# Performance work log

Hardware: AMD Instinct MI355X
Metric: run time of the kernel (lower is better)

Reference implementation:

```python
import jax, jax.numpy as jnp
import numpy as np

B, TOK, D, H, L = 64, 20, 512, 8, 4
S = 512          # tokens per half
HD = D // H
ODIM = 32        # encoder_output_dim


def _ln(x, g, b):
    m = x.mean(-1, keepdims=True)
    v = ((x - m) ** 2).mean(-1, keepdims=True)
    return (x - m) / jnp.sqrt(v + 1e-5) * g + b


def _alibi_slopes(h):
    # mirrors FlashAttentionBlock.build_alibi_slopes (base=2.0)
    base = 2.0
    return jnp.asarray([1.0 / base ** (i // (h // base)) for i in range(h)], dtype=jnp.float32)


def setup_inputs() -> dict:
    key = jax.random.key(0)
    ks = jax.random.split(key, 16)
    r = lambda i, shape, s=0.02: jax.random.normal(ks[i], shape, jnp.float32) * s
    return {
        'x': jax.random.normal(ks[0], (B, 2 * S * TOK), jnp.float32),
        'in_W': r(1, (TOK, D)), 'in_b': jnp.zeros((D,)),
        'qkv_W': r(2, (L, D, 3 * D)), 'qkv_b': jnp.zeros((L, 3 * D)),
        'ln1_g': jnp.ones((L, D)), 'ln1_b': jnp.zeros((L, D)),
        'ffn_W1': r(3, (L, D, 4 * D)), 'ffn_b1': jnp.zeros((L, 4 * D)),
        'ffn_W2': r(4, (L, 4 * D, D)), 'ffn_b2': jnp.zeros((L, D)),
        'ln2_g': jnp.ones((L, D)), 'ln2_b': jnp.zeros((L, D)),
        'out_W': r(5, (D, ODIM)), 'out_b': jnp.zeros((ODIM,)),
        'd1_W': r(6, (2 * S * ODIM, 256)), 'd1_b': jnp.zeros((256,)),
        'bn1_g': jnp.ones((256,)), 'bn1_b': jnp.zeros((256,)),
        'bn1_m': jnp.zeros((256,)), 'bn1_v': jnp.ones((256,)),
        'd2_W': r(7, (256, 128)), 'd2_b': jnp.zeros((128,)),
        'bn2_g': jnp.ones((128,)), 'bn2_b': jnp.zeros((128,)),
        'bn2_m': jnp.zeros((128,)), 'bn2_v': jnp.ones((128,)),
        'fin_W': r(8, (128, 1)), 'fin_b': jnp.zeros((1,)),
    }


def _forward(x, in_W, in_b, qkv_W, qkv_b, ln1_g, ln1_b, ffn_W1, ffn_b1,
             ffn_W2, ffn_b2, ln2_g, ln2_b, out_W, out_b,
             d1_W, d1_b, bn1_g, bn1_b, bn1_m, bn1_v,
             d2_W, d2_b, bn2_g, bn2_b, bn2_m, bn2_v, fin_W, fin_b):
    slopes = _alibi_slopes(H)                                   # [H]
    pos = jnp.arange(S)
    # non-causal ALiBi bias: -slope * |i - j|, shape [H, S, S]
    bias = -slopes[:, None, None] * jnp.abs(pos[:, None] - pos[None, :]).astype(jnp.float32)
    scale = 1.0 / np.sqrt(HD).astype(np.float32)

    def encode(xh):
        b = xh.shape[0]
        t = xh.reshape(b, S, TOK) @ in_W + in_b                 # [b, S, D]
        for l in range(L):
            res = t
            qkv = (t @ qkv_W[l] + qkv_b[l]).reshape(b, S, 3, H, HD)
            q, k, v = qkv[:, :, 0], qkv[:, :, 1], qkv[:, :, 2]  # [b, S, H, HD]
            scores = jnp.einsum('bqhd,bkhd->bhqk', q, k) * scale + bias[None]
            attn = jax.nn.softmax(scores, axis=-1)
            o = jnp.einsum('bhqk,bkhd->bqhd', attn, v).reshape(b, S, D)
            t = _ln(res + o, ln1_g[l], ln1_b[l])
            res = t
            f = jax.nn.relu(t @ ffn_W1[l] + ffn_b1[l]) @ ffn_W2[l] + ffn_b2[l]
            t = _ln(res + f, ln2_g[l], ln2_b[l])
        return (t @ out_W + out_b).reshape(b, -1)               # [b, S*ODIM]

    half = S * TOK
    h = jnp.concatenate([encode(x[:, :half]), encode(x[:, half:])], axis=-1)
    bn = lambda z, g, bb, m, v: (z - m) / jnp.sqrt(v + 1e-5) * g + bb
    h = bn(jax.nn.relu(h @ d1_W + d1_b), bn1_g, bn1_b, bn1_m, bn1_v)
    h = bn(jax.nn.relu(h @ d2_W + d2_b), bn2_g, bn2_b, bn2_m, bn2_v)
    return (h @ fin_W + fin_b).squeeze(-1)                      # [B]


def reference(x, in_W, in_b, qkv_W, qkv_b, ln1_g, ln1_b, ffn_W1, ffn_b1,
              ffn_W2, ffn_b2, ln2_g, ln2_b, out_W, out_b,
              d1_W, d1_b, bn1_g, bn1_b, bn1_m, bn1_v,
              d2_W, d2_b, bn2_g, bn2_b, bn2_m, bn2_v, fin_W, fin_b):
    return _forward(x, in_W, in_b, qkv_W, qkv_b, ln1_g, ln1_b, ffn_W1, ffn_b1,
                    ffn_W2, ffn_b2, ln2_g, ln2_b, out_W, out_b,
                    d1_W, d1_b, bn1_g, bn1_b, bn1_m, bn1_v,
                    d2_W, d2_b, bn2_g, bn2_b, bn2_m, bn2_v, fin_W, fin_b)
```

## Files before the change

kernel.cpp:

```cpp
#include <hip/hip_runtime.h>

#define DEV __device__ __forceinline__

using bf16x8 = __attribute__((ext_vector_type(8))) __bf16;
using f32x4  = __attribute__((ext_vector_type(4))) float;
using u16x8  = __attribute__((ext_vector_type(8))) unsigned short;
using u16x4  = __attribute__((ext_vector_type(4))) unsigned short;

DEV unsigned short f2bf(float f) {
  unsigned u = __builtin_bit_cast(unsigned, f);
  u += 0x7fffu + ((u >> 16) & 1u);
  return (unsigned short)(u >> 16);
}
DEV float bf2f(unsigned short h) {
  unsigned u = ((unsigned)h) << 16;
  return __builtin_bit_cast(float, u);
}
DEV f32x4 mfma16(u16x8 a, u16x8 b, f32x4 c) {
  return __builtin_amdgcn_mfma_f32_16x16x32_bf16(
      __builtin_bit_cast(bf16x8, a), __builtin_bit_cast(bf16x8, b), c, 0, 0, 0);
}
DEV f32x4 zero4() { f32x4 z = {0.f, 0.f, 0.f, 0.f}; return z; }

DEV void glds16(const unsigned short* g, unsigned short* l) {
  __builtin_amdgcn_global_load_lds(
      (const __attribute__((address_space(1))) unsigned int*)g,
      (__attribute__((address_space(3))) unsigned int*)l, 16, 0, 0);
}

#define PH_BAR()                          \
  do {                                    \
    __builtin_amdgcn_sched_barrier(0);    \
    __builtin_amdgcn_s_barrier();         \
    __builtin_amdgcn_sched_barrier(0);    \
  } while (0)

enum { EPI_BIAS = 0, EPI_RELU = 1, EPI_OUT = 2 };

template <int EPI>
__global__ __launch_bounds__(512, 2) void gemm32_k(
    const unsigned short* __restrict__ A, const unsigned short* __restrict__ Bt,
    const float* __restrict__ bias, unsigned short* __restrict__ C, int N, int K) {
  __shared__ unsigned short As[2][8192];
  __shared__ unsigned short Bs[2][8192];
  const int tid = threadIdx.x;
  const int lane = tid & 63, wv = tid >> 6;
  const int q = lane >> 4, ln = lane & 15;
  const int wr = wv >> 2, wc = wv & 3;
  const int ln3 = ln & 3;

  const int Nt = gridDim.x, Mt = gridDim.y;
  const int lin = blockIdx.x + Nt * blockIdx.y;
  const int xcd = lin & 7;
  const int j = lin >> 3;
  const int mi = xcd * (Mt >> 3) + j / Nt;
  const int ni = j % Nt;
  const int m0 = mi << 8, n0 = ni << 8;

  f32x4 acc[8][4];
#pragma unroll
  for (int i = 0; i < 8; ++i)
#pragma unroll
    for (int jj = 0; jj < 4; ++jj) acc[i][jj] = zero4();

  const int sr = lane >> 2;
  const int sc = ((lane & 3) ^ (sr & 3)) << 3;
  const unsigned short* Abase = A + (size_t)(m0 + wv * 16 + sr) * K + sc;
  const unsigned short* Bbase = Bt + (size_t)(n0 + wv * 16 + sr) * K + sc;

  const int T = K >> 5;

  auto stA = [&](int buf, int t) {
    unsigned short* d = &As[buf][wv * 512];
    const unsigned short* s = Abase + t * 32;
    glds16(s, d);
    glds16(s + (size_t)128 * K, d + 4096);
  };
  auto stB = [&](int buf, int t) {
    unsigned short* d = &Bs[buf][wv * 512];
    const unsigned short* s = Bbase + t * 32;
    glds16(s, d);
    glds16(s + (size_t)128 * K, d + 4096);
  };

  stA(0, 0);
  stB(0, 0);
  if (T > 1) {
    stA(1, 1);
    stB(1, 1);
    asm volatile("s_waitcnt vmcnt(4)" ::: "memory");
  } else {
    asm volatile("s_waitcnt vmcnt(0)" ::: "memory");
  }
  PH_BAR();

  for (int u = 0; u < T; ++u) {
    const int cur = u & 1;
    const unsigned short* Ab = &As[cur][0];
    const unsigned short* Bb = &Bs[cur][0];
    u16x8 a0[4], a1[4], b0[4];

#pragma unroll
    for (int mt = 0; mt < 4; ++mt)
      a0[mt] = *(const u16x8*)(Ab + (wr * 128 + mt * 16 + ln) * 32 + ((q ^ ln3) << 3));
#pragma unroll
    for (int nt = 0; nt < 4; ++nt)
      b0[nt] = *(const u16x8*)(Bb + (wc * 64 + nt * 16 + ln) * 32 + ((q ^ ln3) << 3));
    PH_BAR();
    __builtin_amdgcn_s_setprio(1);
#pragma unroll
    for (int nt = 0; nt < 4; ++nt)
#pragma unroll
      for (int mt = 0; mt < 4; ++mt) acc[mt][nt] = mfma16(a0[mt], b0[nt], acc[mt][nt]);
    __builtin_amdgcn_s_setprio(0);
    PH_BAR();

#pragma unroll
    for (int mt = 0; mt < 4; ++mt)
      a1[mt] = *(const u16x8*)(Ab + (wr * 128 + (mt + 4) * 16 + ln) * 32 + ((q ^ ln3) << 3));
    if (u + 2 < T) stB(cur, u + 2);
    PH_BAR();
    __builtin_amdgcn_s_setprio(1);
#pragma unroll
    for (int nt = 0; nt < 4; ++nt)
#pragma unroll
      for (int mt = 0; mt < 4; ++mt)
        acc[mt + 4][nt] = mfma16(a1[mt], b0[nt], acc[mt + 4][nt]);
    __builtin_amdgcn_s_setprio(0);
    PH_BAR();

    if (u + 1 < T) {
      if (u + 2 < T) {
        stA(cur, u + 2);
        asm volatile("s_waitcnt vmcnt(4)" ::: "memory");
      } else {
        asm volatile("s_waitcnt vmcnt(0)" ::: "memory");
      }
      PH_BAR();
    }
  }

#pragma unroll
  for (int mt = 0; mt < 8; ++mt) {
    const int rowb = m0 + wr * 128 + mt * 16 + q * 4;
#pragma unroll
    for (int nt = 0; nt < 4; ++nt) {
      const int col = n0 + wc * 64 + nt * 16 + ln;
      const float bs = bias[col];
#pragma unroll
      for (int r = 0; r < 4; ++r) {
        float v = acc[mt][nt][r] + bs;
        if (EPI == EPI_RELU) v = fmaxf(v, 0.f);
        C[(size_t)(rowb + r) * N + col] = f2bf(v);
      }
    }
  }
}

template <int EPI>
__global__ __launch_bounds__(256) void gemm_k(
    const unsigned short* __restrict__ A, const unsigned short* __restrict__ Bt,
    const float* __restrict__ bias, unsigned short* __restrict__ C, int N, int K) {
  __shared__ unsigned short As[128 * 64];
  __shared__ unsigned short Bs[128 * 64];
  const int tid = threadIdx.x;
  const int lane = tid & 63, wv = tid >> 6;
  const int q = lane >> 4, ln = lane & 15;
  const int wr = wv >> 1, wc = wv & 1;

  const int Nt = gridDim.x, Mt = gridDim.y;
  const int lin = blockIdx.x + Nt * blockIdx.y;
  const int xcd = lin & 7;
  const int j = lin >> 3;
  const int mi = xcd * (Mt >> 3) + j / Nt;
  const int ni = j % Nt;
  const int m0 = mi << 7, n0 = ni << 7;

  f32x4 acc[4][4];
#pragma unroll
  for (int i = 0; i < 4; ++i)
#pragma unroll
    for (int jj = 0; jj < 4; ++jj) acc[i][jj] = zero4();

  const int ra = lane >> 3;
  const int ca = ((lane & 7) ^ ra) << 3;
  const unsigned short* Ap = A + (size_t)(m0 + wv * 32 + ra) * K + ca;
  const unsigned short* Bp = Bt + (size_t)(n0 + wv * 32 + ra) * K + ca;
  unsigned short* AsW = As + wv * 2048;
  unsigned short* BsW = Bs + wv * 2048;
  const int ln7 = ln & 7;

  for (int kb = 0; kb < K; kb += 64) {
    __syncthreads();
#pragma unroll
    for (int t = 0; t < 4; ++t) {
      glds16(Ap + (size_t)(t * 8) * K + kb, AsW + t * 512);
      glds16(Bp + (size_t)(t * 8) * K + kb, BsW + t * 512);
    }
    __syncthreads();
#pragma unroll
    for (int kk = 0; kk < 2; ++kk) {
      const int c = kk * 4 + q;
      const int lo = ln * 64 + ((c ^ ln7) << 3);
      u16x8 af[4];
#pragma unroll
      for (int mt = 0; mt < 4; ++mt)
        af[mt] = *(const u16x8*)(As + (wr * 64 + mt * 16) * 64 + lo);
#pragma unroll
      for (int nt = 0; nt < 4; ++nt) {
        u16x8 bf = *(const u16x8*)(Bs + (wc * 64 + nt * 16) * 64 + lo);
#pragma unroll
        for (int mt = 0; mt < 4; ++mt) acc[mt][nt] = mfma16(af[mt], bf, acc[mt][nt]);
      }
    }
  }

#pragma unroll
  for (int mt = 0; mt < 4; ++mt) {
    const int rowb = m0 + wr * 64 + mt * 16 + q * 4;
#pragma unroll
    for (int nt = 0; nt < 4; ++nt) {
      const int col = n0 + wc * 64 + nt * 16 + ln;
      if (EPI == EPI_OUT && col >= 32) continue;
      const float bs = bias[col];
      const int ldc = (EPI == EPI_OUT) ? 32 : N;
#pragma unroll
      for (int r = 0; r < 4; ++r) {
        float v = acc[mt][nt][r] + bs;
        if (EPI == EPI_RELU) v = fmaxf(v, 0.f);
        C[(size_t)(rowb + r) * ldc + col] = f2bf(v);
      }
    }
  }
}

__global__ __launch_bounds__(256) void vt_k(const unsigned short* __restrict__ big,
                                            unsigned short* __restrict__ vt) {
  __shared__ unsigned short td[64 * 72];
  const int tid = threadIdx.x;
  const int sh = blockIdx.x;
  const int seq = sh >> 3, h = sh & 7;
  const int kt = blockIdx.y;
  {
    const int key = tid >> 2, hdc = (tid & 3) << 4;
    const unsigned short* src =
        big + ((size_t)seq * 512 + kt * 64 + key) * 1536 + 1024 + h * 64 + hdc;
    *(u16x8*)(td + key * 72 + hdc) = *(const u16x8*)src;
    *(u16x8*)(td + key * 72 + hdc + 8) = *(const u16x8*)(src + 8);
  }
  __syncthreads();
  {
    const int hd = tid >> 2, kc = (tid & 3) << 4;
    u16x8 a, b;
#pragma unroll
    for (int j = 0; j < 8; ++j) a[j] = td[(kc + j) * 72 + hd];
#pragma unroll
    for (int j = 0; j < 8; ++j) b[j] = td[(kc + 8 + j) * 72 + hd];
    unsigned short* dst = vt + ((size_t)sh * 64 + hd) * 512 + kt * 64 + kc;
    *(u16x8*)dst = a;
    *(u16x8*)(dst + 8) = b;
  }
}

__global__ __launch_bounds__(256) void attn_k(const unsigned short* __restrict__ qkv,
                                              const unsigned short* __restrict__ vt,
                                              unsigned short* __restrict__ o) {
  __shared__ unsigned short Qs[128 * 72];
  __shared__ unsigned short Ks[2][64 * 64];
  __shared__ unsigned short Vts[2][64 * 64];
  unsigned short* Ps = Qs;
  const int tid = threadIdx.x;
  const int lane = tid & 63, w = tid >> 6, q = lane >> 4, ln = lane & 15;
  const int bh = blockIdx.x;
  const int seq = bh >> 3, h = bh & 7;
  const int qt = blockIdx.y;
  const size_t tokb = (size_t)seq * 512;
  const int qoff = h * 64, koff = 512 + h * 64;
  const float c1 = 0.125f * 1.44269504f;
  const float c2 = ((h < 4) ? 1.0f : 0.5f) * 1.44269504f;

#pragma unroll
  for (int p = 0; p < 4; ++p) {
    int c = p * 256 + tid;
    int row = c >> 3, cc = (c & 7) << 3;
    u16x8 v = *(const u16x8*)(qkv + (tokb + qt * 128 + row) * 1536 + qoff + cc);
    *(u16x8*)(Qs + row * 72 + cc) = v;
  }

  const int sr = lane >> 3;
  const int sc = ((lane & 7) ^ sr) << 3;
  const unsigned short* Kp = qkv + (tokb + w * 16 + sr) * 1536 + koff + sc;
  const unsigned short* Vp = vt + ((size_t)bh * 64 + w * 16 + sr) * 512 + sc;
  const int ln7 = ln & 7;

  auto stage = [&](int kt, int buf) {
    unsigned short* KsW = &Ks[buf][w * 1024];
    unsigned short* VsW = &Vts[buf][w * 1024];
    glds16(Kp + (size_t)(kt * 64) * 1536, KsW);
    glds16(Kp + (size_t)(kt * 64 + 8) * 1536, KsW + 512);
    glds16(Vp + kt * 64, VsW);
    glds16(Vp + kt * 64 + (size_t)8 * 512, VsW + 512);
  };

  stage(0, 0);

  __syncthreads();
  u16x8 aq[2][2];
#pragma unroll
  for (int mt = 0; mt < 2; ++mt)
#pragma unroll
    for (int kc = 0; kc < 2; ++kc)
      aq[mt][kc] = *(const u16x8*)(Qs + (w * 32 + mt * 16 + ln) * 72 + kc * 32 + q * 8);

  float lacc[2] = {0.f, 0.f};
  f32x4 o_acc[2][4];
#pragma unroll
  for (int mt = 0; mt < 2; ++mt)
#pragma unroll
    for (int ht = 0; ht < 4; ++ht) o_acc[mt][ht] = zero4();

  for (int kt = 0; kt < 8; ++kt) {
    const int buf = kt & 1;
    __syncthreads();
    if (kt + 1 < 8) {
      stage(kt + 1, buf ^ 1);
      asm volatile("s_waitcnt vmcnt(4)" ::: "memory");
    } else {
      asm volatile("s_waitcnt vmcnt(0)" ::: "memory");
    }
    __builtin_amdgcn_sched_barrier(0);
    __builtin_amdgcn_s_barrier();
    __builtin_amdgcn_sched_barrier(0);

    f32x4 sacc[2][4];
#pragma unroll
    for (int mt = 0; mt < 2; ++mt)
#pragma unroll
      for (int nt = 0; nt < 4; ++nt) sacc[mt][nt] = zero4();
#pragma unroll
    for (int nt = 0; nt < 4; ++nt)
#pragma unroll
      for (int kc = 0; kc < 2; ++kc) {
        u16x8 bk = *(const u16x8*)(&Ks[buf][(nt * 16 + ln) * 64 + (((kc * 4 + q) ^ ln7) << 3)]);
#pragma unroll
        for (int mt = 0; mt < 2; ++mt) sacc[mt][nt] = mfma16(bk, aq[mt][kc], sacc[mt][nt]);
      }

    const float qp0 = (float)(qt * 128 + w * 32 + ln);
    const float kb0 = (float)(kt * 64 + q * 4);
#pragma unroll
    for (int mt = 0; mt < 2; ++mt) {
      const float qpm = qp0 + (float)(mt * 16);
#pragma unroll
      for (int nt = 0; nt < 4; ++nt) {
        const float kp = kb0 + (float)(nt * 16);
        u16x4 pk;
#pragma unroll
        for (int r = 0; r < 4; ++r) {
          const float ad = fabsf(qpm - (kp + (float)r));
          const float p = exp2f(fmaf(sacc[mt][nt][r], c1, -c2 * ad));
          const unsigned u = __builtin_bit_cast(unsigned, p);
          const unsigned short pb = (unsigned short)((u + 0x8000u) >> 16);
          pk[r] = pb;
          lacc[mt] += bf2f(pb);
        }
        *(u16x4*)(Ps + (w * 32 + mt * 16 + ln) * 72 + nt * 16 + q * 4) = pk;
      }
    }
#pragma unroll
    for (int kc = 0; kc < 2; ++kc) {
      u16x8 pa[2];
#pragma unroll
      for (int mt = 0; mt < 2; ++mt)
        pa[mt] = *(const u16x8*)(Ps + (w * 32 + mt * 16 + ln) * 72 + kc * 32 + q * 8);
#pragma unroll
      for (int ht = 0; ht < 4; ++ht) {
        u16x8 bv = *(const u16x8*)(&Vts[buf][(ht * 16 + ln) * 64 + (((kc * 4 + q) ^ ln7) << 3)]);
#pragma unroll
        for (int mt = 0; mt < 2; ++mt) o_acc[mt][ht] = mfma16(pa[mt], bv, o_acc[mt][ht]);
      }
    }
  }

  float rl[2][4];
#pragma unroll
  for (int mt = 0; mt < 2; ++mt) {
    float l = lacc[mt];
    l += __shfl_xor(l, 16, 64);
    l += __shfl_xor(l, 32, 64);
    const int sb = (lane >> 4) * 20;
#pragma unroll
    for (int r = 0; r < 4; ++r) rl[mt][r] = 1.0f / __shfl(l, sb + r, 64);
  }

#pragma unroll
  for (int mt = 0; mt < 2; ++mt)
#pragma unroll
    for (int ht = 0; ht < 4; ++ht)
#pragma unroll
      for (int r = 0; r < 4; ++r) {
        const int row = qt * 128 + w * 32 + mt * 16 + q * 4 + r;
        const float val = o_acc[mt][ht][r] * rl[mt][r];
        o[(tokb + row) * 512 + h * 64 + ht * 16 + ln] = f2bf(val);
      }
}

__global__ __launch_bounds__(256) void ln_k(const unsigned short* res,
                                            const unsigned short* __restrict__ y,
                                            const float* __restrict__ g,
                                            const float* __restrict__ b,
                                            unsigned short* out) {
  const int lane = threadIdx.x & 63, wv = threadIdx.x >> 6;
  const size_t row = (size_t)blockIdx.x * 4 + wv;
  const size_t base = row * 512 + lane * 8;
  u16x8 rv = *(const u16x8*)(res + base);
  u16x8 yv = *(const u16x8*)(y + base);
  float v[8];
  float s = 0.f, s2 = 0.f;
#pragma unroll
  for (int i = 0; i < 8; ++i) {
    v[i] = bf2f(rv[i]) + bf2f(yv[i]);
    s += v[i];
    s2 += v[i] * v[i];
  }
#pragma unroll
  for (int m = 1; m < 64; m <<= 1) {
    s += __shfl_xor(s, m, 64);
    s2 += __shfl_xor(s2, m, 64);
  }
  const float mean = s * (1.f / 512.f);
  const float var = s2 * (1.f / 512.f) - mean * mean;
  const float rstd = rsqrtf(var + 1e-5f);
  const int c = lane * 8;
  u16x8 ov;
#pragma unroll
  for (int i = 0; i < 8; ++i) ov[i] = f2bf((v[i] - mean) * rstd * g[c + i] + b[c + i]);
  *(u16x8*)(out + base) = ov;
}

__global__ __launch_bounds__(256) void transpose_w(const float* __restrict__ in,
                                                   unsigned short* __restrict__ out,
                                                   int Kin, int Nin, int Kout, int Nout) {
  __shared__ float tile[32][33];
  const int nb = blockIdx.x * 32, kb = blockIdx.y * 32;
  const int tx = threadIdx.x & 31, ty = threadIdx.x >> 5;
#pragma unroll
  for (int i = 0; i < 32; i += 8) {
    int k = kb + ty + i, n = nb + tx;
    tile[ty + i][tx] = (k < Kin && n < Nin) ? in[(size_t)k * Nin + n] : 0.f;
  }
  __syncthreads();
#pragma unroll
  for (int i = 0; i < 32; i += 8) {
    int n = nb + ty + i, k = kb + tx;
    if (n < Nout && k < Kout) out[(size_t)n * Kout + k] = f2bf(tile[tx][ty + i]);
  }
}

__global__ __launch_bounds__(256) void xpad_k(const float* __restrict__ x,
                                              unsigned short* __restrict__ xp) {
  const int idx = blockIdx.x * 256 + threadIdx.x;
  const int tok = idx >> 6, k = idx & 63;
  const int seq = tok >> 9, s = tok & 511;
  const int hf = seq >> 6, b = seq & 63;
  float v = 0.f;
  if (k < 20) v = x[(size_t)b * 20480 + hf * 10240 + s * 20 + k];
  xp[idx] = f2bf(v);
}

__global__ __launch_bounds__(256) void d1_part(const unsigned short* __restrict__ enc,
                                               const float* __restrict__ W,
                                               float* __restrict__ pz) {
  __shared__ float ef[64 * 128];
  const int tid = threadIdx.x;
  const int kb = blockIdx.x * 128;
  const int hf = kb >> 14;
  const int j0 = kb & 16383;
  {
    const int m = tid >> 2, c = (tid & 3) * 32;
    const unsigned short* src = enc + (size_t)hf * 1048576 + (size_t)m * 16384 + j0 + c;
#pragma unroll
    for (int i = 0; i < 4; ++i) {
      u16x8 v = *(const u16x8*)(src + i * 8);
#pragma unroll
      for (int jj = 0; jj < 8; ++jj) ef[m * 128 + c + i * 8 + jj] = bf2f(v[jj]);
    }
  }
  __syncthreads();
  const int n = tid;
  float acc[64];
#pragma unroll
  for (int m = 0; m < 64; ++m) acc[m] = 0.f;
  for (int kc = 0; kc < 128; kc += 4) {
    const float w0 = W[(size_t)(kb + kc) * 256 + n];
    const float w1 = W[(size_t)(kb + kc + 1) * 256 + n];
    const float w2 = W[(size_t)(kb + kc + 2) * 256 + n];
    const float w3 = W[(size_t)(kb + kc + 3) * 256 + n];
#pragma unroll
    for (int m = 0; m < 64; ++m) {
      const f32x4 e = *(const f32x4*)(ef + m * 128 + kc);
      acc[m] += e[0] * w0 + e[1] * w1 + e[2] * w2 + e[3] * w3;
    }
  }
#pragma unroll
  for (int m = 0; m < 64; ++m)
    pz[(size_t)(blockIdx.x * 64 + m) * 256 + n] = acc[m];
}

__global__ __launch_bounds__(256) void d1_fin(const float* __restrict__ pz,
                                              const float* __restrict__ d1b,
                                              const float* __restrict__ g,
                                              const float* __restrict__ b,
                                              const float* __restrict__ mm,
                                              const float* __restrict__ vv,
                                              float* __restrict__ h1) {
  const int m = blockIdx.x, n = threadIdx.x;
  float a = d1b[n];
  for (int sl = 0; sl < 256; ++sl) a += pz[(size_t)(sl * 64 + m) * 256 + n];
  a = fmaxf(a, 0.f);
  a = (a - mm[n]) * rsqrtf(vv[n] + 1e-5f) * g[n] + b[n];
  h1[m * 256 + n] = a;
}

__global__ __launch_bounds__(128) void d2_k(const float* __restrict__ h1,
                                            const float* __restrict__ W,
                                            const float* __restrict__ bb,
                                            const float* __restrict__ g,
                                            const float* __restrict__ b,
                                            const float* __restrict__ mm,
                                            const float* __restrict__ vv,
                                            float* __restrict__ h2) {
  __shared__ float hs[256];
  const int m = blockIdx.x, n = threadIdx.x;
  hs[n] = h1[m * 256 + n];
  hs[n + 128] = h1[m * 256 + n + 128];
  __syncthreads();
  float a = bb[n];
#pragma unroll 8
  for (int k = 0; k < 256; ++k) a += hs[k] * W[k * 128 + n];
  a = fmaxf(a, 0.f);
  a = (a - mm[n]) * rsqrtf(vv[n] + 1e-5f) * g[n] + b[n];
  h2[m * 128 + n] = a;
}

__global__ __launch_bounds__(64) void fin_k(const float* __restrict__ h2,
                                            const float* __restrict__ W,
                                            const float* __restrict__ fb,
                                            float* __restrict__ out) {
  const int m = threadIdx.x;
  float a = fb[0];
#pragma unroll 8
  for (int k = 0; k < 128; ++k) a += h2[m * 128 + k] * W[k];
  out[m] = a;
}

extern "C" void kernel_launch(void* const* d_in, const int* in_sizes, int n_in,
                              void* d_out, int out_size, void* d_ws, size_t ws_size,
                              hipStream_t stream) {
  const float* x      = (const float*)d_in[0];
  const float* in_W   = (const float*)d_in[1];
  const float* in_b   = (const float*)d_in[2];
  const float* qkv_W  = (const float*)d_in[3];
  const float* qkv_b  = (const float*)d_in[4];
  const float* ln1_g  = (const float*)d_in[5];
  const float* ln1_b  = (const float*)d_in[6];
  const float* ffn_W1 = (const float*)d_in[7];
  const float* ffn_b1 = (const float*)d_in[8];
  const float* ffn_W2 = (const float*)d_in[9];
  const float* ffn_b2 = (const float*)d_in[10];
  const float* ln2_g  = (const float*)d_in[11];
  const float* ln2_b  = (const float*)d_in[12];
  const float* out_W  = (const float*)d_in[13];
  const float* out_b  = (const float*)d_in[14];
  const float* d1W    = (const float*)d_in[15];
  const float* d1b    = (const float*)d_in[16];
  const float* bn1g   = (const float*)d_in[17];
  const float* bn1b   = (const float*)d_in[18];
  const float* bn1m   = (const float*)d_in[19];
  const float* bn1v   = (const float*)d_in[20];
  const float* d2W    = (const float*)d_in[21];
  const float* d2b    = (const float*)d_in[22];
  const float* bn2g   = (const float*)d_in[23];
  const float* bn2b   = (const float*)d_in[24];
  const float* bn2m   = (const float*)d_in[25];
  const float* bn2v   = (const float*)d_in[26];
  const float* finW   = (const float*)d_in[27];
  const float* finb   = (const float*)d_in[28];
  (void)in_sizes; (void)n_in; (void)out_size; (void)ws_size;

  char* ws = (char*)d_ws;
  size_t off = 0;
  auto alloc = [&](size_t bytes) {
    char* p = ws + off;
    off += (bytes + 255) & ~(size_t)255;
    return p;
  };
  unsigned short* t     = (unsigned short*)alloc(32768ull * 512 * 2);
  unsigned short* big   = (unsigned short*)alloc(32768ull * 2048 * 2);
  unsigned short* ob    = (unsigned short*)alloc(32768ull * 512 * 2);
  unsigned short* xpad  = (unsigned short*)alloc(65536ull * 64 * 2);
  unsigned short* enc   = (unsigned short*)alloc(65536ull * 32 * 2);
  unsigned short* inWt  = (unsigned short*)alloc(512ull * 64 * 2);
  unsigned short* qkvWt = (unsigned short*)alloc(4ull * 1536 * 512 * 2);
  unsigned short* f1Wt  = (unsigned short*)alloc(4ull * 2048 * 512 * 2);
  unsigned short* f2Wt  = (unsigned short*)alloc(4ull * 512 * 2048 * 2);
  unsigned short* outWt = (unsigned short*)alloc(128ull * 512 * 2);
  float* h1 = (float*)alloc(64ull * 256 * 4);
  float* h2 = (float*)alloc(64ull * 128 * 4);
  float* pz = (float*)big;
  unsigned short* vtb = big + (size_t)32768 * 1536;

  xpad_k<<<16384, 256, 0, stream>>>(x, xpad);
  transpose_w<<<dim3(16, 2), 256, 0, stream>>>(in_W, inWt, 20, 512, 64, 512);
  transpose_w<<<dim3(4, 16), 256, 0, stream>>>(out_W, outWt, 512, 32, 512, 128);
  for (int l = 0; l < 4; ++l) {
    transpose_w<<<dim3(48, 16), 256, 0, stream>>>(qkv_W + (size_t)l * 512 * 1536,
                                                  qkvWt + (size_t)l * 1536 * 512, 512, 1536, 512, 1536);
    transpose_w<<<dim3(64, 16), 256, 0, stream>>>(ffn_W1 + (size_t)l * 512 * 2048,
                                                  f1Wt + (size_t)l * 2048 * 512, 512, 2048, 512, 2048);
    transpose_w<<<dim3(16, 64), 256, 0, stream>>>(ffn_W2 + (size_t)l * 2048 * 512,
                                                  f2Wt + (size_t)l * 512 * 2048, 2048, 512, 2048, 512);
  }

  for (int hf = 0; hf < 2; ++hf) {
    gemm32_k<EPI_BIAS><<<dim3(2, 128), 512, 0, stream>>>(xpad + (size_t)hf * 32768 * 64, inWt, in_b, t, 512, 64);
    for (int l = 0; l < 4; ++l) {
      gemm32_k<EPI_BIAS><<<dim3(6, 128), 512, 0, stream>>>(t, qkvWt + (size_t)l * 1536 * 512,
                                                           qkv_b + l * 1536, big, 1536, 512);
      vt_k<<<dim3(512, 8), 256, 0, stream>>>(big, vtb);
      attn_k<<<dim3(512, 4), 256, 0, stream>>>(big, vtb, ob);
      ln_k<<<8192, 256, 0, stream>>>(t, ob, ln1_g + l * 512, ln1_b + l * 512, t);
      gemm32_k<EPI_RELU><<<dim3(8, 128), 512, 0, stream>>>(t, f1Wt + (size_t)l * 2048 * 512,
                                                           ffn_b1 + l * 2048, big, 2048, 512);
      gemm32_k<EPI_BIAS><<<dim3(2, 128), 512, 0, stream>>>(big, f2Wt + (size_t)l * 512 * 2048,
                                                           ffn_b2 + l * 512, ob, 512, 2048);
      ln_k<<<8192, 256, 0, stream>>>(t, ob, ln2_g + l * 512, ln2_b + l * 512, t);
    }
    gemm_k<EPI_OUT><<<dim3(1, 256), 256, 0, stream>>>(t, outWt, out_b,
                                                      enc + (size_t)hf * 32768 * 32, 128, 512);
  }

  d1_part<<<256, 256, 0, stream>>>(enc, d1W, pz);
  d1_fin<<<64, 256, 0, stream>>>(pz, d1b, bn1g, bn1b, bn1m, bn1v, h1);
  d2_k<<<64, 128, 0, stream>>>(h1, d2W, d2b, bn2g, bn2b, bn2m, bn2v, h2);
  fin_k<<<1, 64, 0, stream>>>(h2, finW, finb, (float*)d_out);
}
```

Before: 3.364 ms.

## Fuse V transpose into QKV GEMM epilogue and change LDS swizzle

The QKV projection GEMM now writes the V columns straight into the transposed per-head layout the attention kernel expects. This removes the separate vt_k transpose launch and its extra global read and write of V. The LDS swizzle in gemm32_k also changes to XOR with bits 1-2 of the row index instead of bits 0-1, meant to reduce bank conflicts on the fragment reads. The V epilogue stores are 4-element column-strided writes, which coalesce worse than the original row-major stores.

```diff
diff --git a/kernel.cpp b/kernel.cpp
--- a/kernel.cpp
+++ b/kernel.cpp
@@ -35,19 +35,20 @@
     __builtin_amdgcn_sched_barrier(0);    \
   } while (0)
 
-enum { EPI_BIAS = 0, EPI_RELU = 1, EPI_OUT = 2 };
+enum { EPI_BIAS = 0, EPI_RELU = 1, EPI_OUT = 2, EPI_QKV = 3 };
 
 template <int EPI>
 __global__ __launch_bounds__(512, 2) void gemm32_k(
     const unsigned short* __restrict__ A, const unsigned short* __restrict__ Bt,
-    const float* __restrict__ bias, unsigned short* __restrict__ C, int N, int K) {
+    const float* __restrict__ bias, unsigned short* __restrict__ C,
+    unsigned short* __restrict__ Cv, int N, int K) {
   __shared__ unsigned short As[2][8192];
   __shared__ unsigned short Bs[2][8192];
   const int tid = threadIdx.x;
   const int lane = tid & 63, wv = tid >> 6;
   const int q = lane >> 4, ln = lane & 15;
   const int wr = wv >> 2, wc = wv & 3;
-  const int ln3 = ln & 3;
+  const int sw = ((q ^ ((ln >> 1) & 3)) << 3);
 
   const int Nt = gridDim.x, Mt = gridDim.y;
   const int lin = blockIdx.x + Nt * blockIdx.y;
@@ -64,7 +65,7 @@
     for (int jj = 0; jj < 4; ++jj) acc[i][jj] = zero4();
 
   const int sr = lane >> 2;
-  const int sc = ((lane & 3) ^ (sr & 3)) << 3;
+  const int sc = ((lane & 3) ^ ((lane >> 3) & 3)) << 3;
   const unsigned short* Abase = A + (size_t)(m0 + wv * 16 + sr) * K + sc;
   const unsigned short* Bbase = Bt + (size_t)(n0 + wv * 16 + sr) * K + sc;
 
@@ -102,10 +103,10 @@
 
 #pragma unroll
     for (int mt = 0; mt < 4; ++mt)
-      a0[mt] = *(const u16x8*)(Ab + (wr * 128 + mt * 16 + ln) * 32 + ((q ^ ln3) << 3));
+      a0[mt] = *(const u16x8*)(Ab + (wr * 128 + mt * 16 + ln) * 32 + sw);
 #pragma unroll
     for (int nt = 0; nt < 4; ++nt)
-      b0[nt] = *(const u16x8*)(Bb + (wc * 64 + nt * 16 + ln) * 32 + ((q ^ ln3) << 3));
+      b0[nt] = *(const u16x8*)(Bb + (wc * 64 + nt * 16 + ln) * 32 + sw);
     PH_BAR();
     __builtin_amdgcn_s_setprio(1);
 #pragma unroll
@@ -117,7 +118,7 @@
 
 #pragma unroll
     for (int mt = 0; mt < 4; ++mt)
-      a1[mt] = *(const u16x8*)(Ab + (wr * 128 + (mt + 4) * 16 + ln) * 32 + ((q ^ ln3) << 3));
+      a1[mt] = *(const u16x8*)(Ab + (wr * 128 + (mt + 4) * 16 + ln) * 32 + sw);
     if (u + 2 < T) stB(cur, u + 2);
     PH_BAR();
     __builtin_amdgcn_s_setprio(1);
@@ -143,15 +144,24 @@
 #pragma unroll
   for (int mt = 0; mt < 8; ++mt) {
     const int rowb = m0 + wr * 128 + mt * 16 + q * 4;
+    const int seq = rowb >> 9, key0 = rowb & 511;
 #pragma unroll
     for (int nt = 0; nt < 4; ++nt) {
       const int col = n0 + wc * 64 + nt * 16 + ln;
       const float bs = bias[col];
-#pragma unroll
-      for (int r = 0; r < 4; ++r) {
-        float v = acc[mt][nt][r] + bs;
-        if (EPI == EPI_RELU) v = fmaxf(v, 0.f);
-        C[(size_t)(rowb + r) * N + col] = f2bf(v);
+      if (EPI == EPI_QKV && n0 >= 1024) {
+        const int hh = (col - 1024) >> 6, hd = col & 63;
+        u16x4 pk;
+#pragma unroll
+        for (int r = 0; r < 4; ++r) pk[r] = f2bf(acc[mt][nt][r] + bs);
+        *(u16x4*)(Cv + ((size_t)((seq * 8 + hh) * 64 + hd)) * 512 + key0) = pk;
+      } else {
+#pragma unroll
+        for (int r = 0; r < 4; ++r) {
+          float v = acc[mt][nt][r] + bs;
+          if (EPI == EPI_RELU) v = fmaxf(v, 0.f);
+          C[(size_t)(rowb + r) * N + col] = f2bf(v);
+        }
       }
     }
   }
@@ -231,34 +241,6 @@
         C[(size_t)(rowb + r) * ldc + col] = f2bf(v);
       }
     }
-  }
-}
-
-__global__ __launch_bounds__(256) void vt_k(const unsigned short* __restrict__ big,
-                                            unsigned short* __restrict__ vt) {
-  __shared__ unsigned short td[64 * 72];
-  const int tid = threadIdx.x;
-  const int sh = blockIdx.x;
-  const int seq = sh >> 3, h = sh & 7;
-  const int kt = blockIdx.y;
-  {
-    const int key = tid >> 2, hdc = (tid & 3) << 4;
-    const unsigned short* src =
-        big + ((size_t)seq * 512 + kt * 64 + key) * 1536 + 1024 + h * 64 + hdc;
-    *(u16x8*)(td + key * 72 + hdc) = *(const u16x8*)src;
-    *(u16x8*)(td + key * 72 + hdc + 8) = *(const u16x8*)(src + 8);
-  }
-  __syncthreads();
-  {
-    const int hd = tid >> 2, kc = (tid & 3) << 4;
-    u16x8 a, b;
-#pragma unroll
-    for (int j = 0; j < 8; ++j) a[j] = td[(kc + j) * 72 + hd];
-#pragma unroll
-    for (int j = 0; j < 8; ++j) b[j] = td[(kc + 8 + j) * 72 + hd];
-    unsigned short* dst = vt + ((size_t)sh * 64 + hd) * 512 + kt * 64 + kc;
-    *(u16x8*)dst = a;
-    *(u16x8*)(dst + 8) = b;
   }
 }
 
@@ -623,17 +605,16 @@
   }
 
   for (int hf = 0; hf < 2; ++hf) {
-    gemm32_k<EPI_BIAS><<<dim3(2, 128), 512, 0, stream>>>(xpad + (size_t)hf * 32768 * 64, inWt, in_b, t, 512, 64);
+    gemm32_k<EPI_BIAS><<<dim3(2, 128), 512, 0, stream>>>(xpad + (size_t)hf * 32768 * 64, inWt, in_b, t, nullptr, 512, 64);
     for (int l = 0; l < 4; ++l) {
-      gemm32_k<EPI_BIAS><<<dim3(6, 128), 512, 0, stream>>>(t, qkvWt + (size_t)l * 1536 * 512,
-                                                           qkv_b + l * 1536, big, 1536, 512);
-      vt_k<<<dim3(512, 8), 256, 0, stream>>>(big, vtb);
+      gemm32_k<EPI_QKV><<<dim3(6, 128), 512, 0, stream>>>(t, qkvWt + (size_t)l * 1536 * 512,
+                                                          qkv_b + l * 1536, big, vtb, 1536, 512);
       attn_k<<<dim3(512, 4), 256, 0, stream>>>(big, vtb, ob);
       ln_k<<<8192, 256, 0, stream>>>(t, ob, ln1_g + l * 512, ln1_b + l * 512, t);
       gemm32_k<EPI_RELU><<<dim3(8, 128), 512, 0, stream>>>(t, f1Wt + (size_t)l * 2048 * 512,
-                                                           ffn_b1 + l * 2048, big, 2048, 512);
+                                                           ffn_b1 + l * 2048, big, nullptr, 2048, 512);
       gemm32_k<EPI_BIAS><<<dim3(2, 128), 512, 0, stream>>>(big, f2Wt + (size_t)l * 512 * 2048,
-                                                           ffn_b2 + l * 512, ob, 512, 2048);
+                                                           ffn_b2 + l * 512, ob, nullptr, 512, 2048);
       ln_k<<<8192, 256, 0, stream>>>(t, ob, ln2_g + l * 512, ln2_b + l * 512, t);
     }
     gemm_k<EPI_OUT><<<dim3(1, 256), 256, 0, stream>>>(t, outWt, out_b,
```

Measured after the change: 3.223 ms. 4.2% less time.
